# Kernel optimization log

Hardware: AMD Instinct MI355X
Metric: run time of the kernel (lower is better)

The kernel has to match this reference:

```python
import jax, jax.numpy as jnp
import numpy as np
import math

D_MODEL = 2048
NUM_HEADS = 16
D_HEAD = D_MODEL // NUM_HEADS
ROPE_BASE = 10000.0

def _rope(t, pos):
    # t: [b, h, T, d_head]; standard rotate-half RoPE with base 10000.
    T, d = t.shape[-2], t.shape[-1]
    start = max(pos, 0)  # pos < 0 means training / position 0
    inv_freq = 1.0 / (ROPE_BASE ** (jnp.arange(0, d, 2, dtype=jnp.float32) / d))  # [d/2]
    positions = jnp.arange(start, start + T, dtype=jnp.float32)                   # [T]
    ang = positions[:, None] * inv_freq[None, :]                                  # [T, d/2]
    cos, sin = jnp.cos(ang), jnp.sin(ang)
    x1, x2 = t[..., : d // 2], t[..., d // 2 :]
    return jnp.concatenate([x1 * cos - x2 * sin, x1 * sin + x2 * cos], axis=-1)

def setup_inputs() -> dict:
    key = jax.random.key(0)
    kx, kq, kk, kv, kw = jax.random.split(key, 5)
    s = 1.0 / math.sqrt(D_MODEL)
    return {
        "x": jax.random.normal(kx, (2, 2048, D_MODEL), dtype=jnp.float32),
        "q_out": jax.random.normal(kq, (D_MODEL, D_MODEL), dtype=jnp.float32) * s,
        "k_out": jax.random.normal(kk, (D_MODEL, D_MODEL), dtype=jnp.float32) * s,
        "v_out": jax.random.normal(kv, (D_MODEL, D_MODEL), dtype=jnp.float32) * s,
        "w_out": jax.random.normal(kw, (D_MODEL, D_MODEL), dtype=jnp.float32) * s,
        "pos": 0,
    }

def reference(x, q_out, k_out, v_out, w_out, pos):
    b, t, d = x.shape
    h, dh = NUM_HEADS, D_HEAD

    def heads(y):  # [b, t, d] -> [b, h, t, dh]
        return y.reshape(b, t, h, dh).transpose(0, 2, 1, 3)

    q = _rope(heads(jnp.einsum('btd,de->bte', x, q_out)), pos)
    k = _rope(heads(jnp.einsum('btd,de->bte', x, k_out)), pos)
    v = heads(jnp.einsum('btd,de->bte', x, v_out))

    score = jnp.einsum('bhqd,bhkd->bhqk', q, k) / math.sqrt(dh)
    causal = jnp.triu(jnp.ones((t, t), dtype=bool), k=1)  # True above diagonal -> masked
    score = jnp.where(causal, -jnp.inf, score)
    weights = jax.nn.softmax(score, axis=-1)
    ctx = jnp.einsum('bhqk,bhkd->bhqd', weights, v)        # [b, h, t, dh]
    ctx = ctx.transpose(0, 2, 1, 3).reshape(b, t, d)
    return jnp.einsum('btd,de->bte', ctx, w_out)
```

## Files before the change

### kernel.cpp

```cpp
#include <hip/hip_runtime.h>
#include <hip/hip_bf16.h>
#include <math.h>

#define NH 16
#define DH 128
#define DM 2048
#define BB 2
#define TT 2048

typedef unsigned short u16;
typedef __attribute__((ext_vector_type(8))) __bf16 bf16x8;
typedef __attribute__((ext_vector_type(8))) u16 u16x8;
typedef __attribute__((ext_vector_type(4))) u16 u16x4;
typedef __attribute__((ext_vector_type(4))) float f32x4;

__device__ __forceinline__ float bf2f(u16 a){
  union { unsigned u; float f; } v; v.u = ((unsigned)a) << 16; return v.f;
}
__device__ __forceinline__ u16 f2bf(float f){
  union { float f; unsigned u; } v; v.f = f;
  unsigned r = v.u + 0x7fffu + ((v.u >> 16) & 1u);
  return (u16)(r >> 16);
}

typedef const __attribute__((address_space(1))) unsigned int* gas_p;
typedef __attribute__((address_space(3))) unsigned int* las_p;
__device__ __forceinline__ void gl_lds16(const u16* g, u16* lds_uniform_base){
  __builtin_amdgcn_global_load_lds((gas_p)(const void*)g,
                                   (las_p)(void*)lds_uniform_base, 16, 0, 0);
}

#define SB() do{ asm volatile("" ::: "memory"); \
                 __builtin_amdgcn_s_barrier();  \
                 asm volatile("" ::: "memory"); }while(0)
#define WAITV4 asm volatile("s_waitcnt vmcnt(4)" ::: "memory")
#define WAITV0 asm volatile("s_waitcnt vmcnt(0)" ::: "memory")

__global__ __launch_bounds__(256)
void cvt_f32_bf16(const float* __restrict__ src, u16* __restrict__ dst, int n4){
  const int i = blockIdx.x * 256 + threadIdx.x;
  if (i >= n4) return;
  const f32x4 v = *(const f32x4*)(src + (size_t)i * 4);
  u16x4 o;
  #pragma unroll
  for (int j = 0; j < 4; j++) o[j] = f2bf(v[j]);
  *(u16x4*)(dst + (size_t)i * 4) = o;
}

__global__ __launch_bounds__(256)
void transpose2048(const float* __restrict__ W, u16* __restrict__ Wt){
  __shared__ u16 tile[32][33];
  const int tx = threadIdx.x, ty = threadIdx.y;
  const int bx = blockIdx.x * 32, by = blockIdx.y * 32;
  #pragma unroll
  for (int i = 0; i < 32; i += 8)
    tile[ty + i][tx] = f2bf(W[(size_t)(by + ty + i) * DM + bx + tx]);
  __syncthreads();
  #pragma unroll
  for (int i = 0; i < 32; i += 8)
    Wt[(size_t)(bx + ty + i) * DM + by + tx] = tile[tx][ty + i];
}

__global__ __launch_bounds__(256)
void transpose3(const float* __restrict__ w0, const float* __restrict__ w1,
                const float* __restrict__ w2, u16* __restrict__ dst){
  __shared__ u16 tile[32][33];
  const int z = blockIdx.z;
  const float* W = (z == 0) ? w0 : (z == 1) ? w1 : w2;
  u16* Wt = dst + (size_t)z * DM * DM;
  const int tx = threadIdx.x, ty = threadIdx.y;
  const int bx = blockIdx.x * 32, by = blockIdx.y * 32;
  #pragma unroll
  for (int i = 0; i < 32; i += 8)
    tile[ty + i][tx] = f2bf(W[(size_t)(by + ty + i) * DM + bx + tx]);
  __syncthreads();
  #pragma unroll
  for (int i = 0; i < 32; i += 8)
    Wt[(size_t)(bx + ty + i) * DM + by + tx] = tile[tx][ty + i];
}

__global__ __launch_bounds__(256)
void gemm_bt(const u16* __restrict__ A, const u16* __restrict__ Bt_base,
             void* __restrict__ C0, u16* __restrict__ Ck, u16* __restrict__ Cv,
             int mode0){
  __shared__ u16 As[2][128][32];
  __shared__ u16 Bs[2][128][32];
  const int z = blockIdx.z;
  const u16* Bt = Bt_base + (size_t)z * DM * DM;
  void* C = (z == 0) ? C0 : (z == 1) ? (void*)Ck : (void*)Cv;
  const int mode = (z == 0) ? mode0 : (z == 1) ? 3 : 2;

  const int tid = threadIdx.x;
  const int wave = tid >> 6, lane = tid & 63;
  const int wm = wave & 1, wn = wave >> 1;
  const int row16 = lane & 15, quad = lane >> 4;
  const int m0 = blockIdx.x * 128, n0 = blockIdx.y * 128;

  const f32x4 zero = {0.f, 0.f, 0.f, 0.f};
  f32x4 acc[4][4];
  #pragma unroll
  for (int i = 0; i < 4; i++)
    #pragma unroll
    for (int j = 0; j < 4; j++) acc[i][j] = zero;

  const int srow = lane >> 2;
  const int scol = (lane & 3) * 8;

  for (int k0 = 0; k0 < DM; k0 += 64){
    #pragma unroll
    for (int c = 0; c < 2; c++){
      const int rbase = wave * 32 + c * 16;
      const u16* pa = A  + (size_t)(m0 + rbase + srow) * DM + k0 + scol;
      const u16* pb = Bt + (size_t)(n0 + rbase + srow) * DM + k0 + scol;
      gl_lds16(pa,      &As[0][rbase][0]);
      gl_lds16(pa + 32, &As[1][rbase][0]);
      gl_lds16(pb,      &Bs[0][rbase][0]);
      gl_lds16(pb + 32, &Bs[1][rbase][0]);
    }
    __syncthreads();
    #pragma unroll
    for (int buf = 0; buf < 2; buf++){
      bf16x8 af[4], bfr[4];
      #pragma unroll
      for (int mt = 0; mt < 4; mt++)
        af[mt] = *(const bf16x8*)&As[buf][wm * 64 + mt * 16 + row16][quad * 8];
      #pragma unroll
      for (int nt = 0; nt < 4; nt++)
        bfr[nt] = *(const bf16x8*)&Bs[buf][wn * 64 + nt * 16 + row16][quad * 8];
      #pragma unroll
      for (int mt = 0; mt < 4; mt++)
        #pragma unroll
        for (int nt = 0; nt < 4; nt++)
          acc[mt][nt] = __builtin_amdgcn_mfma_f32_16x16x32_bf16(af[mt], bfr[nt], acc[mt][nt], 0, 0, 0);
    }
    __syncthreads();
  }

  #pragma unroll
  for (int mt = 0; mt < 4; mt++){
    #pragma unroll
    for (int nt = 0; nt < 4; nt++){
      #pragma unroll
      for (int r = 0; r < 4; r++){
        const int m = m0 + wm * 64 + mt * 16 + quad * 4 + r;
        const int n = n0 + wn * 64 + nt * 16 + row16;
        const int b = m >> 11, t = m & (TT - 1);
        const int hh = n >> 7, dh = n & (DH - 1);
        if (mode == 1){
          ((u16*)C)[(((size_t)(b * NH + hh) * TT + t) * DH) + dh] = f2bf(acc[mt][nt][r]);
        } else if (mode == 3){
          const int dhs = dh ^ ((t & 7) << 3);
          ((u16*)C)[(((size_t)(b * NH + hh) * TT + t) * DH) + dhs] = f2bf(acc[mt][nt][r]);
        } else if (mode == 2){
          const int ts = (t & 63) ^ ((dh & 7) << 3);
          ((u16*)C)[(((size_t)(b * NH + hh) * 32 + (t >> 6)) * 8192) + dh * 64 + ts] = f2bf(acc[mt][nt][r]);
        } else {
          ((float*)C)[(size_t)m * DM + n] = acc[mt][nt][r];
        }
      }
    }
  }
}

__global__ __launch_bounds__(256)
void gemm_bt2(const u16* __restrict__ A, const u16* __restrict__ Bt_base,
              void* __restrict__ C0, u16* __restrict__ Ck, u16* __restrict__ Cv,
              int mode0){
  __shared__ u16 As[2][128][32];
  __shared__ u16 Bs[2][128][32];
  const int z = blockIdx.z;
  const u16* Bt = Bt_base + (size_t)z * DM * DM;
  void* C = (z == 0) ? C0 : (z == 1) ? (void*)Ck : (void*)Cv;
  const int mode = (z == 0) ? mode0 : (z == 1) ? 3 : 2;

  const int tid = threadIdx.x;
  const int wave = tid >> 6, lane = tid & 63;
  const int wm = wave & 1, wn = wave >> 1;
  const int row16 = lane & 15, quad = lane >> 4;
  const int m0 = blockIdx.x * 128, n0 = blockIdx.y * 128;

  const f32x4 zero = {0.f, 0.f, 0.f, 0.f};
  f32x4 acc[4][4];
  #pragma unroll
  for (int i = 0; i < 4; i++)
    #pragma unroll
    for (int j = 0; j < 4; j++) acc[i][j] = zero;

  const int srow = lane >> 2;
  const int scol = ((lane & 3) ^ ((lane >> 3) & 3)) * 8;
  const u16* aBase = A  + (size_t)(m0 + wave * 32 + srow) * DM + scol;
  const u16* bBase = Bt + (size_t)(n0 + wave * 32 + srow) * DM + scol;

  const int fcol = (quad ^ ((row16 >> 1) & 3)) * 8;

  #define STAGE2(kh, kc) do{ \
    const int ko = (kc) + (kh) * 32; \
    gl_lds16(aBase + ko,                     &As[kh][wave * 32][0]); \
    gl_lds16(aBase + ko + (size_t)16 * DM,   &As[kh][wave * 32 + 16][0]); \
    gl_lds16(bBase + ko,                     &Bs[kh][wave * 32][0]); \
    gl_lds16(bBase + ko + (size_t)16 * DM,   &Bs[kh][wave * 32 + 16][0]); \
  }while(0)

  #define PHASE2(kh) do{ \
    bf16x8 af[4], bk[4]; \
    _Pragma("unroll") \
    for (int mt = 0; mt < 4; mt++) \
      af[mt] = *(const bf16x8*)&As[kh][wm * 64 + mt * 16 + row16][fcol]; \
    _Pragma("unroll") \
    for (int nt = 0; nt < 4; nt++) \
      bk[nt] = *(const bf16x8*)&Bs[kh][wn * 64 + nt * 16 + row16][fcol]; \
    __builtin_amdgcn_s_setprio(1); \
    _Pragma("unroll") \
    for (int mt = 0; mt < 4; mt++) \
      _Pragma("unroll") \
      for (int nt = 0; nt < 4; nt++) \
        acc[mt][nt] = __builtin_amdgcn_mfma_f32_16x16x32_bf16(af[mt], bk[nt], acc[mt][nt], 0, 0, 0); \
    __builtin_amdgcn_s_setprio(0); \
  }while(0)

  STAGE2(0, 0);

  for (int t = 0; t < 31; ++t){
    const int kc = t * 64;
    STAGE2(1, kc);
    WAITV4;
    SB();
    PHASE2(0);
    SB();
    STAGE2(0, kc + 64);
    WAITV4;
    SB();
    PHASE2(1);
    SB();
  }
  STAGE2(1, 31 * 64);
  WAITV4; SB();
  PHASE2(0);
  SB();
  WAITV0; SB();
  PHASE2(1);

  #undef STAGE2
  #undef PHASE2

  #pragma unroll
  for (int mt = 0; mt < 4; mt++){
    #pragma unroll
    for (int nt = 0; nt < 4; nt++){
      #pragma unroll
      for (int r = 0; r < 4; r++){
        const int m = m0 + wm * 64 + mt * 16 + quad * 4 + r;
        const int n = n0 + wn * 64 + nt * 16 + row16;
        const int b = m >> 11, t = m & (TT - 1);
        const int hh = n >> 7, dh = n & (DH - 1);
        if (mode == 1){
          ((u16*)C)[(((size_t)(b * NH + hh) * TT + t) * DH) + dh] = f2bf(acc[mt][nt][r]);
        } else if (mode == 3){
          const int dhs = dh ^ ((t & 7) << 3);
          ((u16*)C)[(((size_t)(b * NH + hh) * TT + t) * DH) + dhs] = f2bf(acc[mt][nt][r]);
        } else if (mode == 2){
          const int ts = (t & 63) ^ ((dh & 7) << 3);
          ((u16*)C)[(((size_t)(b * NH + hh) * 32 + (t >> 6)) * 8192) + dh * 64 + ts] = f2bf(acc[mt][nt][r]);
        } else {
          ((float*)C)[(size_t)m * DM + n] = acc[mt][nt][r];
        }
      }
    }
  }
}

__global__ __launch_bounds__(256)
void rope2(u16* __restrict__ qb, u16* __restrict__ kb, const int* __restrict__ posp){
  const int idx = blockIdx.x * 256 + threadIdx.x;
  const int pair = idx & 63;
  const int row = idx >> 6;
  const int t = row & (TT - 1);
  int p0 = *posp; if (p0 < 0) p0 = 0;
  const float tf = (float)(p0 + t);
  const size_t base = (size_t)row * DH;
  {
    const float inv = expf(-(float)pair * (9.2103403719761836f / 64.f));
    float sn, cs; sincosf(tf * inv, &sn, &cs);
    const float q1 = bf2f(qb[base + pair]);
    const float q2 = bf2f(qb[base + 64 + pair]);
    qb[base + pair]      = f2bf(q1 * cs - q2 * sn);
    qb[base + 64 + pair] = f2bf(q1 * sn + q2 * cs);
  }
  {
    const int pl = pair ^ ((t & 7) << 3);
    const float inv = expf(-(float)pl * (9.2103403719761836f / 64.f));
    float sn, cs; sincosf(tf * inv, &sn, &cs);
    const float k1 = bf2f(kb[base + pair]);
    const float k2 = bf2f(kb[base + 64 + pair]);
    kb[base + pair]      = f2bf(k1 * cs - k2 * sn);
    kb[base + 64 + pair] = f2bf(k1 * sn + k2 * cs);
  }
}

template<bool MASK>
__device__ __forceinline__ void attn_tile(
    int kt0, int qbase, int wave, int row16, int quad,
    const bf16x8 (&qf)[4],
    u16 (&k_s)[64][128], u16 (&vt_s)[128][64], u16 (&p_s)[4][16][72],
    f32x4 (&o_acc)[8], float (&l_acc)[4])
{
  const float scale = 0.08838834764831845f;
  const f32x4 zero = {0.f, 0.f, 0.f, 0.f};
  const int fx = (row16 & 7) << 3;
  f32x4 s_acc[4];
  #pragma unroll
  for (int nt = 0; nt < 4; nt++) s_acc[nt] = zero;
  #pragma unroll
  for (int st = 0; st < 4; st++)
    #pragma unroll
    for (int nt = 0; nt < 4; nt++){
      const bf16x8 kf = *(const bf16x8*)&k_s[nt * 16 + row16][(st * 32 + quad * 8) ^ fx];
      s_acc[nt] = __builtin_amdgcn_mfma_f32_16x16x32_bf16(qf[st], kf, s_acc[nt], 0, 0, 0);
    }
  #pragma unroll
  for (int r = 0; r < 4; r++){
    float ps = 0.f;
    #pragma unroll
    for (int nt = 0; nt < 4; nt++){
      float p = __expf(s_acc[nt][r] * scale);
      if (MASK){
        const int qr = qbase + quad * 4 + r;
        if (kt0 + nt * 16 + row16 > qr) p = 0.f;
      }
      ps += p;
      p_s[wave][quad * 4 + r][nt * 16 + row16] = f2bf(p);
    }
    l_acc[r] += ps;
  }
  asm volatile("" ::: "memory");

  #pragma unroll
  for (int kk = 0; kk < 2; kk++){
    const bf16x8 pf = *(const bf16x8*)&p_s[wave][row16][kk * 32 + quad * 8];
    #pragma unroll
    for (int nd = 0; nd < 8; nd++){
      const bf16x8 vb = *(const bf16x8*)&vt_s[nd * 16 + row16][(kk * 32 + quad * 8) ^ fx];
      o_acc[nd] = __builtin_amdgcn_mfma_f32_16x16x32_bf16(pf, vb, o_acc[nd], 0, 0, 0);
    }
  }
}

__global__ __launch_bounds__(256)
void attn_fwd(const u16* __restrict__ q, const u16* __restrict__ k,
              const u16* __restrict__ vtg, u16* __restrict__ ctx){
  __shared__ u16 k_s[64][128];
  __shared__ u16 vt_s[128][64];
  __shared__ u16 p_s[4][16][72];
  const int tid = threadIdx.x;
  const int wave = tid >> 6, lane = tid & 63;
  const int row16 = lane & 15, quad = lane >> 4;
  const int bh = blockIdx.y;
  const int q0 = (31 - blockIdx.x) * 64;
  const int qbase = q0 + wave * 16;
  const size_t bho = (size_t)bh * TT * DH;

  bf16x8 qf[4];
  {
    const u16* qp = q + bho + (size_t)(qbase + row16) * DH + quad * 8;
    #pragma unroll
    for (int st = 0; st < 4; st++) qf[st] = *(const bf16x8*)(qp + st * 32);
  }

  float l_acc[4] = {0.f, 0.f, 0.f, 0.f};
  const f32x4 zero = {0.f, 0.f, 0.f, 0.f};
  f32x4 o_acc[8];
  #pragma unroll
  for (int i = 0; i < 8; i++) o_acc[i] = zero;

  const int kl_r = lane >> 4, kl_c = (lane & 15) * 8;
  const int vl_r = lane >> 3, vl_c = (lane & 7) * 8;

  for (int kt0 = 0; kt0 < q0 + 64; kt0 += 64){
    #pragma unroll
    for (int i = 0; i < 4; i++){
      const int rb = wave * 16 + i * 4;
      gl_lds16(k + bho + (size_t)(kt0 + rb + kl_r) * DH + kl_c, &k_s[rb][0]);
    }
    const u16* vpan = vtg + ((size_t)bh * 32 + (kt0 >> 6)) * 8192;
    #pragma unroll
    for (int i = 0; i < 4; i++){
      const int rb = wave * 32 + i * 8;
      gl_lds16(vpan + (size_t)(rb + vl_r) * 64 + vl_c, &vt_s[rb][0]);
    }
    __syncthreads();

    if (kt0 < q0)
      attn_tile<false>(kt0, qbase, wave, row16, quad, qf, k_s, vt_s, p_s, o_acc, l_acc);
    else
      attn_tile<true >(kt0, qbase, wave, row16, quad, qf, k_s, vt_s, p_s, o_acc, l_acc);

    __syncthreads();
  }

  #pragma unroll
  for (int r = 0; r < 4; r++){
    #pragma unroll
    for (int off = 1; off < 16; off <<= 1) l_acc[r] += __shfl_xor(l_acc[r], off, 64);
  }

  const int b = bh >> 4, h = bh & 15;
  #pragma unroll
  for (int nd = 0; nd < 8; nd++){
    #pragma unroll
    for (int r = 0; r < 4; r++){
      const int qr = qbase + quad * 4 + r;
      const size_t off = ((size_t)b * TT + qr) * DM + h * DH + nd * 16 + row16;
      ctx[off] = f2bf(o_acc[nd][r] / l_acc[r]);
    }
  }
}

extern "C" void kernel_launch(void* const* d_in, const int* in_sizes, int n_in,
                              void* d_out, int out_size, void* d_ws, size_t ws_size,
                              hipStream_t stream){
  const float* x  = (const float*)d_in[0];
  const float* wq = (const float*)d_in[1];
  const float* wk = (const float*)d_in[2];
  const float* wv = (const float*)d_in[3];
  const float* wo = (const float*)d_in[4];
  const int* pos  = (const int*)d_in[5];

  char* ws = (char*)d_ws;
  const dim3 tg(64, 64), tb(32, 8);

  if (ws_size >= 92274688ull){
    u16* xb  = (u16*)ws;                  u16* cb = xb;
    u16* wt3 = (u16*)(ws + 16777216);
    u16* qb  = (u16*)(ws + 41943040);
    u16* kb  = (u16*)(ws + 58720256);
    u16* vtg = (u16*)(ws + 75497472);

    cvt_f32_bf16<<<8192, 256, 0, stream>>>(x, xb, 2097152);
    transpose3<<<dim3(64, 64, 3), tb, 0, stream>>>(wq, wk, wv, wt3);
    gemm_bt2<<<dim3(32, 16, 3), 256, 0, stream>>>(xb, wt3, qb, kb, vtg, 1);
    transpose2048<<<tg, tb, 0, stream>>>(wo, wt3);
    rope2<<<16384, 256, 0, stream>>>(qb, kb, pos);
    attn_fwd<<<dim3(32, 32), 256, 0, stream>>>(qb, kb, vtg, cb);
    gemm_bt2<<<dim3(32, 16, 1), 256, 0, stream>>>(cb, wt3, d_out, 0, 0, 0);
  } else {
    u16* xb  = (u16*)ws;                  u16* cb = xb;
    u16* wt  = (u16*)(ws + 16777216);
    u16* qb  = (u16*)(ws + 25165824);
    u16* kb  = (u16*)(ws + 41943040);
    u16* vtg = (u16*)(ws + 58720256);

    cvt_f32_bf16<<<8192, 256, 0, stream>>>(x, xb, 2097152);
    transpose2048<<<tg, tb, 0, stream>>>(wq, wt);
    gemm_bt<<<dim3(32, 16, 1), 256, 0, stream>>>(xb, wt, qb, 0, 0, 1);
    transpose2048<<<tg, tb, 0, stream>>>(wk, wt);
    gemm_bt<<<dim3(32, 16, 1), 256, 0, stream>>>(xb, wt, kb, 0, 0, 3);
    transpose2048<<<tg, tb, 0, stream>>>(wv, wt);
    gemm_bt<<<dim3(32, 16, 1), 256, 0, stream>>>(xb, wt, vtg, 0, 0, 2);
    rope2<<<16384, 256, 0, stream>>>(qb, kb, pos);
    attn_fwd<<<dim3(32, 32), 256, 0, stream>>>(qb, kb, vtg, cb);
    transpose2048<<<tg, tb, 0, stream>>>(wo, wt);
    gemm_bt<<<dim3(32, 16, 1), 256, 0, stream>>>(cb, wt, d_out, 0, 0, 0);
  }
}
```

Baseline: 475.9 us.

## Restructure GEMM pipeline to 64-wide K stages and prioritize attention MFMAs

The projection GEMM now stages a full 64-element K slice per buffer, using an XOR swizzle over 8 column groups. Its double-buffered loop issues the next global-to-LDS load before computing the current buffer, which needs one barrier per iteration instead of four. The attention tile raises wave priority around its two MFMA blocks. The aim is to cut barrier and wait overhead and keep the matrix units busy, at the cost of twice the LDS per block and a full vmcnt(0) wait each iteration.

```diff
diff --git a/kernel.cpp b/kernel.cpp
--- a/kernel.cpp
+++ b/kernel.cpp
@@ -33,7 +33,6 @@
 #define SB() do{ asm volatile("" ::: "memory"); \
                  __builtin_amdgcn_s_barrier();  \
                  asm volatile("" ::: "memory"); }while(0)
-#define WAITV4 asm volatile("s_waitcnt vmcnt(4)" ::: "memory")
 #define WAITV0 asm volatile("s_waitcnt vmcnt(0)" ::: "memory")
 
 __global__ __launch_bounds__(256)
@@ -163,11 +162,11 @@
 }
 
 __global__ __launch_bounds__(256)
-void gemm_bt2(const u16* __restrict__ A, const u16* __restrict__ Bt_base,
+void gemm_bt4(const u16* __restrict__ A, const u16* __restrict__ Bt_base,
               void* __restrict__ C0, u16* __restrict__ Ck, u16* __restrict__ Cv,
               int mode0){
-  __shared__ u16 As[2][128][32];
-  __shared__ u16 Bs[2][128][32];
+  __shared__ u16 As[2][128][64];
+  __shared__ u16 Bs[2][128][64];
   const int z = blockIdx.z;
   const u16* Bt = Bt_base + (size_t)z * DM * DM;
   void* C = (z == 0) ? C0 : (z == 1) ? (void*)Ck : (void*)Cv;
@@ -186,62 +185,55 @@
     #pragma unroll
     for (int j = 0; j < 4; j++) acc[i][j] = zero;
 
-  const int srow = lane >> 2;
-  const int scol = ((lane & 3) ^ ((lane >> 3) & 3)) * 8;
-  const u16* aBase = A  + (size_t)(m0 + wave * 32 + srow) * DM + scol;
-  const u16* bBase = Bt + (size_t)(n0 + wave * 32 + srow) * DM + scol;
-
-  const int fcol = (quad ^ ((row16 >> 1) & 3)) * 8;
-
-  #define STAGE2(kh, kc) do{ \
-    const int ko = (kc) + (kh) * 32; \
-    gl_lds16(aBase + ko,                     &As[kh][wave * 32][0]); \
-    gl_lds16(aBase + ko + (size_t)16 * DM,   &As[kh][wave * 32 + 16][0]); \
-    gl_lds16(bBase + ko,                     &Bs[kh][wave * 32][0]); \
-    gl_lds16(bBase + ko + (size_t)16 * DM,   &Bs[kh][wave * 32 + 16][0]); \
+  const int sr = lane >> 3;
+  const int sc = ((lane & 7) ^ sr) * 8;
+  const u16* aBase = A  + (size_t)(m0 + wave * 32 + sr) * DM + sc;
+  const u16* bBase = Bt + (size_t)(n0 + wave * 32 + sr) * DM + sc;
+
+  #define STG4(bf, k0) do{ \
+    _Pragma("unroll") \
+    for (int j = 0; j < 4; j++){ \
+      gl_lds16(aBase + (size_t)(j * 8) * DM + (k0), &As[bf][wave * 32 + j * 8][0]); \
+      gl_lds16(bBase + (size_t)(j * 8) * DM + (k0), &Bs[bf][wave * 32 + j * 8][0]); \
+    } \
   }while(0)
 
-  #define PHASE2(kh) do{ \
-    bf16x8 af[4], bk[4]; \
+  #define CMP4(bf) do{ \
+    bf16x8 af[2][4], bk[2][4]; \
     _Pragma("unroll") \
-    for (int mt = 0; mt < 4; mt++) \
-      af[mt] = *(const bf16x8*)&As[kh][wm * 64 + mt * 16 + row16][fcol]; \
-    _Pragma("unroll") \
-    for (int nt = 0; nt < 4; nt++) \
-      bk[nt] = *(const bf16x8*)&Bs[kh][wn * 64 + nt * 16 + row16][fcol]; \
+    for (int kk = 0; kk < 2; kk++){ \
+      const int pc = ((kk * 4 + quad) ^ (row16 & 7)) * 8; \
+      _Pragma("unroll") \
+      for (int mt = 0; mt < 4; mt++) \
+        af[kk][mt] = *(const bf16x8*)&As[bf][wm * 64 + mt * 16 + row16][pc]; \
+      _Pragma("unroll") \
+      for (int nt = 0; nt < 4; nt++) \
+        bk[kk][nt] = *(const bf16x8*)&Bs[bf][wn * 64 + nt * 16 + row16][pc]; \
+    } \
     __builtin_amdgcn_s_setprio(1); \
     _Pragma("unroll") \
-    for (int mt = 0; mt < 4; mt++) \
+    for (int kk = 0; kk < 2; kk++) \
       _Pragma("unroll") \
-      for (int nt = 0; nt < 4; nt++) \
-        acc[mt][nt] = __builtin_amdgcn_mfma_f32_16x16x32_bf16(af[mt], bk[nt], acc[mt][nt], 0, 0, 0); \
+      for (int mt = 0; mt < 4; mt++) \
+        _Pragma("unroll") \
+        for (int nt = 0; nt < 4; nt++) \
+          acc[mt][nt] = __builtin_amdgcn_mfma_f32_16x16x32_bf16(af[kk][mt], bk[kk][nt], acc[mt][nt], 0, 0, 0); \
     __builtin_amdgcn_s_setprio(0); \
   }while(0)
 
-  STAGE2(0, 0);
+  STG4(0, 0);
+  WAITV0; SB();
 
   for (int t = 0; t < 31; ++t){
-    const int kc = t * 64;
-    STAGE2(1, kc);
-    WAITV4;
+    STG4((t + 1) & 1, (t + 1) * 64);
+    CMP4(t & 1);
+    WAITV0;
     SB();
-    PHASE2(0);
-    SB();
-    STAGE2(0, kc + 64);
-    WAITV4;
-    SB();
-    PHASE2(1);
-    SB();
-  }
-  STAGE2(1, 31 * 64);
-  WAITV4; SB();
-  PHASE2(0);
-  SB();
-  WAITV0; SB();
-  PHASE2(1);
-
-  #undef STAGE2
-  #undef PHASE2
+  }
+  CMP4(1);
+
+  #undef STG4
+  #undef CMP4
 
   #pragma unroll
   for (int mt = 0; mt < 4; mt++){
@@ -310,6 +302,7 @@
   f32x4 s_acc[4];
   #pragma unroll
   for (int nt = 0; nt < 4; nt++) s_acc[nt] = zero;
+  __builtin_amdgcn_s_setprio(1);
   #pragma unroll
   for (int st = 0; st < 4; st++)
     #pragma unroll
@@ -317,6 +310,7 @@
       const bf16x8 kf = *(const bf16x8*)&k_s[nt * 16 + row16][(st * 32 + quad * 8) ^ fx];
       s_acc[nt] = __builtin_amdgcn_mfma_f32_16x16x32_bf16(qf[st], kf, s_acc[nt], 0, 0, 0);
     }
+  __builtin_amdgcn_s_setprio(0);
   #pragma unroll
   for (int r = 0; r < 4; r++){
     float ps = 0.f;
@@ -334,6 +328,7 @@
   }
   asm volatile("" ::: "memory");
 
+  __builtin_amdgcn_s_setprio(1);
   #pragma unroll
   for (int kk = 0; kk < 2; kk++){
     const bf16x8 pf = *(const bf16x8*)&p_s[wave][row16][kk * 32 + quad * 8];
@@ -343,6 +338,7 @@
       o_acc[nd] = __builtin_amdgcn_mfma_f32_16x16x32_bf16(pf, vb, o_acc[nd], 0, 0, 0);
     }
   }
+  __builtin_amdgcn_s_setprio(0);
 }
 
 __global__ __launch_bounds__(256)
@@ -437,11 +433,11 @@
 
     cvt_f32_bf16<<<8192, 256, 0, stream>>>(x, xb, 2097152);
     transpose3<<<dim3(64, 64, 3), tb, 0, stream>>>(wq, wk, wv, wt3);
-    gemm_bt2<<<dim3(32, 16, 3), 256, 0, stream>>>(xb, wt3, qb, kb, vtg, 1);
+    gemm_bt4<<<dim3(32, 16, 3), 256, 0, stream>>>(xb, wt3, qb, kb, vtg, 1);
     transpose2048<<<tg, tb, 0, stream>>>(wo, wt3);
     rope2<<<16384, 256, 0, stream>>>(qb, kb, pos);
     attn_fwd<<<dim3(32, 32), 256, 0, stream>>>(qb, kb, vtg, cb);
-    gemm_bt2<<<dim3(32, 16, 1), 256, 0, stream>>>(cb, wt3, d_out, 0, 0, 0);
+    gemm_bt4<<<dim3(32, 16, 1), 256, 0, stream>>>(cb, wt3, d_out, 0, 0, 0);
   } else {
     u16* xb  = (u16*)ws;                  u16* cb = xb;
     u16* wt  = (u16*)(ws + 16777216);
```

Result: faster. 458.8 us (-3.6%).
